# Performance work log

Measured on AMD Instinct MI355X. Metric: run time of the kernel, lower is better.

## Reference

```python
import jax, jax.numpy as jnp
import numpy as np

# Module hyperparameters (init_kwargs): shape_data = [n_t, n_y, n_x]
N_T, N_Y, N_X = 5, 32, 32
N = N_Y * N_X            # nb_nodes
DX = DY = DT = 1.0


def setup_inputs() -> dict:
    key = jax.random.key(0)
    k1, k2, k3 = jax.random.split(key, 3)
    n_b = 4
    kappa = jax.random.uniform(k1, (n_b, 1, N, N_T), dtype=jnp.float32)
    m = jax.random.normal(k2, (n_b, 2, N, N_T), dtype=jnp.float32)
    H = jax.random.normal(k3, (n_b, 2, 2, N, N_T), dtype=jnp.float32)
    return {"kappa": kappa, "m": m, "H": H}


def _stencil_indices():
    # 9-point stencil on the n_y x n_x grid; row-major node index = y*n_x + x.
    yy, xx = np.meshgrid(np.arange(N_Y), np.arange(N_X), indexing="ij")
    yy, xx = yy.reshape(-1), xx.reshape(-1)
    node = np.arange(N)
    offs = [(0, 0), (0, 1), (0, -1), (1, 0), (-1, 0), (1, 1), (1, -1), (-1, 1), (-1, -1)]
    rows, cols, valid = [], [], []
    for oy, ox in offs:
        ny, nx = yy + oy, xx + ox
        ok = (ny >= 0) & (ny < N_Y) & (nx >= 0) & (nx < N_X)
        rows.append(node)
        cols.append(np.where(ok, ny * N_X + nx, node))
        valid.append(ok.astype(np.float32))
    return (jnp.asarray(np.concatenate(rows)),
            jnp.asarray(np.concatenate(cols)),
            jnp.asarray(np.concatenate(valid)))

ROWS, COLS, VALID = _stencil_indices()


def _build_A(kappa, m, H):
    # Finite-difference discretization of A = kappa^2 I + m.grad - div(H grad)
    # kappa: [b,t,N]; m: [b,t,2,N]; H: [b,t,2,2,N]
    mx, my = m[..., 0, :], m[..., 1, :]
    H11, H22 = H[..., 0, 0, :], H[..., 1, 1, :]
    H12 = 0.5 * (H[..., 0, 1, :] + H[..., 1, 0, :])
    c0 = kappa ** 2 + 2.0 * H11 / DX ** 2 + 2.0 * H22 / DY ** 2   # center
    cpx = mx / (2 * DX) - H11 / DX ** 2                           # (0,+1)
    cmx = -mx / (2 * DX) - H11 / DX ** 2                          # (0,-1)
    cpy = my / (2 * DY) - H22 / DY ** 2                           # (+1,0)
    cmy = -my / (2 * DY) - H22 / DY ** 2                          # (-1,0)
    cc = H12 / (2 * DX * DY)                                      # cross term
    # order matches _stencil_indices offsets
    vals = jnp.concatenate([c0, cpx, cmx, cpy, cmy, -cc, cc, cc, -cc], axis=-1)
    vals = vals * VALID                                           # zero out-of-grid neighbors
    b, t = vals.shape[0], vals.shape[1]
    A = jnp.zeros((b, t, N, N), vals.dtype)
    return A.at[:, :, ROWS, COLS].add(vals)


def reference(kappa, m, H):
    # rearrange to [batch, time, ...] leading
    kap = jnp.transpose(kappa[:, 0], (0, 2, 1))          # [b,t,N]
    mm = jnp.transpose(m, (0, 3, 1, 2))                  # [b,t,2,N]
    HH = jnp.transpose(H, (0, 4, 1, 2, 3))               # [b,t,2,2,N]
    A = _build_A(kap, mm, HH)                            # [b,t,N,N]
    I = jnp.eye(N, dtype=A.dtype)
    M = I + DT * A                                       # M_k = Id + dt * A_k
    MM = jnp.einsum("btij,btjk->btik", M, M)             # spspmm(M_k, M_k)
    b = M.shape[0]
    Q = jnp.zeros((b, N_T * N, N_T * N), A.dtype)
    # block-tridiagonal precision matrix assembly (QR = Id)
    Q = Q.at[:, 0:N, 0:N].set(MM[:, 0])
    Q = Q.at[:, 0:N, N:2 * N].set(-M[:, 1])
    for i in range(1, N_T - 1):
        Q = Q.at[:, i * N:(i + 1) * N, (i - 1) * N:i * N].set(-M[:, i - 1])
        Q = Q.at[:, i * N:(i + 1) * N, i * N:(i + 1) * N].set(MM[:, i] + I)
        Q = Q.at[:, i * N:(i + 1) * N, (i + 1) * N:(i + 2) * N].set(-M[:, i + 1])
    i = N_T - 1
    Q = Q.at[:, i * N:(i + 1) * N, (i - 1) * N:i * N].set(-M[:, i - 1])
    Q = Q.at[:, i * N:(i + 1) * N, i * N:(i + 1) * N].set(MM[:, i])
    return Q
```

## Files before the change

### kernel.cpp

```cpp
#include <hip/hip_runtime.h>

#define NT   5
#define NY   32
#define NX   32
#define NN   1024
#define QDIM 5120
#define NB   4

__device__ const int c_oy[9] = {0, 0, 0, 1, -1, 1, 1, -1, -1};
__device__ const int c_ox[9] = {0, 1, -1, 0, 0, 1, -1, 1, -1};

__device__ __forceinline__ void stencil9(const float* __restrict__ kap,
                                         const float* __restrict__ m,
                                         const float* __restrict__ H,
                                         int b, int t, int n, float s[9]) {
    float k   = kap[((size_t)b * NN + n) * NT + t];
    float mx  = m[(((size_t)b * 2 + 0) * NN + n) * NT + t];
    float my  = m[(((size_t)b * 2 + 1) * NN + n) * NT + t];
    float H11 = H[((((size_t)b * 2 + 0) * 2 + 0) * NN + n) * NT + t];
    float H01 = H[((((size_t)b * 2 + 0) * 2 + 1) * NN + n) * NT + t];
    float H10 = H[((((size_t)b * 2 + 1) * 2 + 0) * NN + n) * NT + t];
    float H22 = H[((((size_t)b * 2 + 1) * 2 + 1) * NN + n) * NT + t];
    float cc = 0.25f * (H01 + H10);
    s[0] = 1.0f + k * k + 2.0f * H11 + 2.0f * H22;
    s[1] =  0.5f * mx - H11;
    s[2] = -0.5f * mx - H11;
    s[3] =  0.5f * my - H22;
    s[4] = -0.5f * my - H22;
    s[5] = -cc;
    s[6] =  cc;
    s[7] =  cc;
    s[8] = -cc;
    int y = n >> 5, x = n & 31;
    if (x == NX - 1) { s[1] = 0.f; s[5] = 0.f; s[7] = 0.f; }
    if (x == 0)      { s[2] = 0.f; s[6] = 0.f; s[8] = 0.f; }
    if (y == NY - 1) { s[3] = 0.f; s[5] = 0.f; s[6] = 0.f; }
    if (y == 0)      { s[4] = 0.f; s[7] = 0.f; s[8] = 0.f; }
}

__global__ __launch_bounds__(64) void spde_scatter(const float* __restrict__ kap,
                                                   const float* __restrict__ m,
                                                   const float* __restrict__ H,
                                                   float* __restrict__ Q) {
    const int oy[9] = {0, 0, 0, 1, -1, 1, 1, -1, -1};
    const int ox[9] = {0, 1, -1, 0, 0, 1, -1, 1, -1};

    int row = blockIdx.x;
    int b = row / (NT * NN);
    int g = row - b * (NT * NN);
    int t = g >> 10;
    int r = g & (NN - 1);
    int ry = r >> 5, rx = r & 31;
    int tid = threadIdx.x;

    __shared__ float sk[9][9];
    __shared__ float moff[2][9];
    __shared__ float accL[25];

    if (tid < 9) {
        int ky = ry + c_oy[tid], kx = rx + c_ox[tid];
        bool valid = ((unsigned)ky < NY) && ((unsigned)kx < NX);
        int k = valid ? (ky * NX + kx) : r;
        float s[9];
        stencil9(kap, m, H, b, t, k, s);
#pragma unroll
        for (int e = 0; e < 9; ++e)
            sk[tid][(oy[e] + 1) * 3 + (ox[e] + 1)] = s[e];
    } else if (tid == 9) {
        float s[9] = {0,0,0,0,0,0,0,0,0};
        if (t >= 1) stencil9(kap, m, H, b, t - 1, r, s);
#pragma unroll
        for (int e = 0; e < 9; ++e) moff[0][e] = -s[e];
    } else if (tid == 10) {
        float s[9] = {0,0,0,0,0,0,0,0,0};
        if (t <= NT - 2) stencil9(kap, m, H, b, t + 1, r, s);
#pragma unroll
        for (int e = 0; e < 9; ++e) moff[1][e] = -s[e];
    }
    __syncthreads();

    if (tid < 25) {
        int dy = tid / 5 - 2, dx = tid % 5 - 2;
        float a = 0.f;
#pragma unroll
        for (int d1 = 0; d1 < 9; ++d1) {
            int dy2 = dy - oy[d1], dx2 = dx - ox[d1];
            if (dy2 >= -1 && dy2 <= 1 && dx2 >= -1 && dx2 <= 1) {
                a += sk[0][(oy[d1] + 1) * 3 + (ox[d1] + 1)]
                   * sk[d1][(dy2 + 1) * 3 + (dx2 + 1)];
            }
        }
        if (tid == 12 && t >= 1 && t <= NT - 2) a += 1.0f;
        accL[tid] = a;
    }
    __syncthreads();

    size_t rowbase = ((size_t)b * QDIM + g) * QDIM;

    if (tid < 25) {
        int dy = tid / 5 - 2, dx = tid % 5 - 2;
        int cy = ry + dy, cx = rx + dx;
        if ((unsigned)cy < NY && (unsigned)cx < NX)
            Q[rowbase + (size_t)t * NN + cy * NX + cx] = accL[tid];
    } else if (tid >= 32 && tid < 41) {
        if (t >= 1) {
            int d = tid - 32;
            int cy = ry + c_oy[d], cx = rx + c_ox[d];
            if ((unsigned)cy < NY && (unsigned)cx < NX)
                Q[rowbase + (size_t)(t - 1) * NN + cy * NX + cx] = moff[0][d];
        }
    } else if (tid >= 48 && tid < 57) {
        if (t <= NT - 2) {
            int d = tid - 48;
            int cy = ry + c_oy[d], cx = rx + c_ox[d];
            if ((unsigned)cy < NY && (unsigned)cx < NX)
                Q[rowbase + (size_t)(t + 1) * NN + cy * NX + cx] = moff[1][d];
        }
    }
}

extern "C" void kernel_launch(void* const* d_in, const int* in_sizes, int n_in,
                              void* d_out, int out_size, void* d_ws, size_t ws_size,
                              hipStream_t stream) {
    const float* kap = (const float*)d_in[0];
    const float* m   = (const float*)d_in[1];
    const float* H   = (const float*)d_in[2];
    float* Q = (float*)d_out;

    hipMemsetAsync(d_out, 0, (size_t)out_size * sizeof(float), stream);

    int nrows = NB * NT * NN;
    spde_scatter<<<nrows, 64, 0, stream>>>(kap, m, H, Q);
}
```

Before: 436.1 us.

## Fuse zero-fill into scatter kernel with full-row vectorized nontemporal stores

After: 412.2 us (median of 2 runs). 5.5% less time.

```diff
diff --git a/kernel.cpp b/kernel.cpp
--- a/kernel.cpp
+++ b/kernel.cpp
@@ -6,6 +6,8 @@
 #define NN   1024
 #define QDIM 5120
 #define NB   4
+
+typedef float vfloat4 __attribute__((ext_vector_type(4)));
 
 __device__ const int c_oy[9] = {0, 0, 0, 1, -1, 1, 1, -1, -1};
 __device__ const int c_ox[9] = {0, 1, -1, 0, 0, 1, -1, 1, -1};
@@ -38,10 +40,10 @@
     if (y == 0)      { s[4] = 0.f; s[7] = 0.f; s[8] = 0.f; }
 }
 
-__global__ __launch_bounds__(64) void spde_scatter(const float* __restrict__ kap,
-                                                   const float* __restrict__ m,
-                                                   const float* __restrict__ H,
-                                                   float* __restrict__ Q) {
+__global__ __launch_bounds__(256) void spde_fused(const float* __restrict__ kap,
+                                                  const float* __restrict__ m,
+                                                  const float* __restrict__ H,
+                                                  float* __restrict__ Q) {
     const int oy[9] = {0, 0, 0, 1, -1, 1, 1, -1, -1};
     const int ox[9] = {0, 1, -1, 0, 0, 1, -1, 1, -1};
 
@@ -53,10 +55,16 @@
     int ry = r >> 5, rx = r & 31;
     int tid = threadIdx.x;
 
+    __shared__ float lds_row[3][NN];
     __shared__ float sk[9][9];
     __shared__ float moff[2][9];
-    __shared__ float accL[25];
 
+    {
+        vfloat4 z4 = {0.f, 0.f, 0.f, 0.f};
+        vfloat4* p = (vfloat4*)&lds_row[0][0];
+#pragma unroll
+        for (int w = 0; w < 3; ++w) p[tid + 256 * w] = z4;
+    }
     if (tid < 9) {
         int ky = ry + c_oy[tid], kx = rx + c_ox[tid];
         bool valid = ((unsigned)ky < NY) && ((unsigned)kx < NX);
@@ -91,31 +99,34 @@
             }
         }
         if (tid == 12 && t >= 1 && t <= NT - 2) a += 1.0f;
-        accL[tid] = a;
-    }
-    __syncthreads();
-
-    size_t rowbase = ((size_t)b * QDIM + g) * QDIM;
-
-    if (tid < 25) {
-        int dy = tid / 5 - 2, dx = tid % 5 - 2;
         int cy = ry + dy, cx = rx + dx;
         if ((unsigned)cy < NY && (unsigned)cx < NX)
-            Q[rowbase + (size_t)t * NN + cy * NX + cx] = accL[tid];
+            lds_row[1][cy * NX + cx] = a;
     } else if (tid >= 32 && tid < 41) {
         if (t >= 1) {
             int d = tid - 32;
             int cy = ry + c_oy[d], cx = rx + c_ox[d];
             if ((unsigned)cy < NY && (unsigned)cx < NX)
-                Q[rowbase + (size_t)(t - 1) * NN + cy * NX + cx] = moff[0][d];
+                lds_row[0][cy * NX + cx] = moff[0][d];
         }
     } else if (tid >= 48 && tid < 57) {
         if (t <= NT - 2) {
             int d = tid - 48;
             int cy = ry + c_oy[d], cx = rx + c_ox[d];
             if ((unsigned)cy < NY && (unsigned)cx < NX)
-                Q[rowbase + (size_t)(t + 1) * NN + cy * NX + cx] = moff[1][d];
+                lds_row[2][cy * NX + cx] = moff[1][d];
         }
+    }
+    __syncthreads();
+
+    float* dst = Q + ((size_t)b * QDIM + g) * QDIM + 4 * tid;
+    const vfloat4* src = (const vfloat4*)&lds_row[0][4 * tid];
+    vfloat4 z4 = {0.f, 0.f, 0.f, 0.f};
+#pragma unroll
+    for (int kk = 0; kk < NT; ++kk) {
+        int z = kk - t + 1;
+        vfloat4 v = ((unsigned)z < 3u) ? src[(size_t)z * (NN / 4)] : z4;
+        __builtin_nontemporal_store(v, (vfloat4*)(dst + (size_t)kk * NN));
     }
 }
 
@@ -127,8 +138,6 @@
     const float* H   = (const float*)d_in[2];
     float* Q = (float*)d_out;
 
-    hipMemsetAsync(d_out, 0, (size_t)out_size * sizeof(float), stream);
-
     int nrows = NB * NT * NN;
-    spde_scatter<<<nrows, 64, 0, stream>>>(kap, m, H, Q);
+    spde_fused<<<nrows, 256, 0, stream>>>(kap, m, H, Q);
 }
```
